# Kernel tuning notes

Hardware: AMD Instinct MI355X
Metric: run time of the kernel (lower is better)

Reference implementation:

```python
import jax, jax.numpy as jnp
import numpy as np

IN_F, OUT_F, RANK, ALPHA, NUM_ADAPTERS = 1024, 1024, 8, 1.0, 8
B, S = 32, 1024
SCALE = ALPHA / RANK


def setup_inputs() -> dict:
    key = jax.random.key(0)
    k1, k2, k3, k4, k5, k6 = jax.random.split(key, 6)
    x = jax.random.normal(k1, (B, S, IN_F), dtype=jnp.float32)
    subject_id = jax.random.randint(k2, (B,), 0, NUM_ADAPTERS)
    # base linear: W [out,in], bias [out] (torch nn.Linear layout)
    W = jax.random.normal(k3, (OUT_F, IN_F), dtype=jnp.float32) * (1.0 / np.sqrt(IN_F))
    b = jax.random.normal(k4, (OUT_F,), dtype=jnp.float32) * 0.01
    # stacked LoRA weights: A [E, rank, in], Bw [E, out, rank]
    # (original inits Bw to zeros; randomized here so the LoRA path is exercised)
    A = jax.random.normal(k5, (NUM_ADAPTERS, RANK, IN_F), dtype=jnp.float32) * 0.02
    Bw = jax.random.normal(k6, (NUM_ADAPTERS, OUT_F, RANK), dtype=jnp.float32) * 0.02
    return {"x": x, "W": W, "b": b, "A": A, "Bw": Bw, "subject_id": subject_id}


def reference(x, W, b, A, Bw, subject_id):
    # base linear: [B,S,O]
    out = jnp.einsum("bsd,od->bso", x, W) + b
    # gather per-batch adapter weights (equivalent to the per-adapter mask loop)
    A_sel = A[subject_id]   # [B, rank, in]
    B_sel = Bw[subject_id]  # [B, out, rank]
    h = jnp.einsum("bsd,brd->bsr", x, A_sel)          # [B,S,rank]
    lora = jnp.einsum("bsr,bor->bso", h, B_sel) * SCALE  # [B,S,out]
    return out + lora
```

## Files before the change

### kernel.cpp

```cpp
#include <hip/hip_runtime.h>
#include <hip/hip_bf16.h>

typedef __bf16 bf16_t;
typedef bf16_t bf16x4 __attribute__((ext_vector_type(4)));
typedef bf16_t bf16x8 __attribute__((ext_vector_type(8)));
typedef float  f32x4  __attribute__((ext_vector_type(4)));

#define IN_F   1024
#define OUT_F  1024
#define RANK   8
#define NE     8
#define BATCH  32
#define SEQ    1024
#define M_TOT  (BATCH * SEQ)
#define SCALE  0.125f
#define NT     16

#define GLOAD_LDS16(g, l)                                                     \
  __builtin_amdgcn_global_load_lds(                                           \
      (const __attribute__((address_space(1))) void*)(g),                     \
      (__attribute__((address_space(3))) void*)(l), 16, 0, 0)

#define CFENCE asm volatile("" ::: "memory")
#define BAR()                                                                 \
  do { CFENCE; __builtin_amdgcn_s_barrier(); CFENCE; } while (0)
#define VMCNT(n) asm volatile("s_waitcnt vmcnt(" #n ")" ::: "memory")
#define LGKM0()  asm volatile("s_waitcnt lgkmcnt(0)" ::: "memory")

__global__ __launch_bounds__(256) void build_weff(
    const float* __restrict__ W, const float* __restrict__ A,
    const float* __restrict__ Bw, bf16_t* __restrict__ weff) {
  const int e  = blockIdx.x >> 10;
  const int o  = blockIdx.x & 1023;
  const int d0 = threadIdx.x << 2;

  f32x4 acc = *(const f32x4*)(W + ((size_t)o << 10) + d0);
  const float* bwr = Bw + (((size_t)e << 10) + o) * RANK;
  const float* ab  = A + (((size_t)e * RANK) << 10) + d0;
#pragma unroll
  for (int r = 0; r < RANK; ++r) {
    const float s = SCALE * bwr[r];
    const f32x4 a4 = *(const f32x4*)(ab + ((size_t)r << 10));
    acc += s * a4;
  }
  bf16x4 ov;
#pragma unroll
  for (int j = 0; j < 4; ++j) ov[j] = (bf16_t)acc[j];
  *(bf16x4*)(weff + (((size_t)e << 10) + o) * IN_F + d0) = ov;
}

__global__ __launch_bounds__(512, 2) void gemm_fused(
    const float* __restrict__ xf, const bf16_t* __restrict__ weff,
    const float* __restrict__ bias, const int* __restrict__ sid,
    float* __restrict__ out) {
  __shared__ bf16_t lds[2][2][2][8192];

  const int bid0 = blockIdx.x;
  const int wgid = ((bid0 & 7) << 6) + (bid0 >> 3);
  const int mb = wgid >> 2, nb = wgid & 3;
  const int m0 = mb << 8, n0 = nb << 8;
  const int e = sid[mb >> 2];

  const int tid = threadIdx.x;
  const int lane = tid & 63, wid = tid >> 6;
  const int wm = wid >> 2, wn = wid & 3;

  const float*  agf   = xf + ((size_t)m0 << 10);
  const bf16_t* bgbase = weff + ((size_t)e << 20) + ((size_t)n0 << 10);

  int soff[2];
#pragma unroll
  for (int i = 0; i < 2; ++i) {
    const int r = (wid << 5) + (i << 4) + (lane >> 2);
    const int sg = (lane & 3) ^ ((r >> 1) & 3);
    soff[i] = (r << 10) + (sg << 3);
  }

  int agoff[4], awoff[4];
  {
    const int c0 = (tid & 7) << 3;
    const int kh = c0 >> 5;
    const int cg = (c0 >> 3) & 3;
#pragma unroll
    for (int q = 0; q < 4; ++q) {
      const int r = (q << 6) + (tid >> 3);
      agoff[q] = (r << 10) + c0;
      const int gs = cg ^ ((r >> 1) & 3);
      awoff[q] = (kh << 13) + (r << 5) + (gs << 3);
    }
  }

  int aoff[8], boff[4];
#pragma unroll
  for (int mi = 0; mi < 8; ++mi) {
    const int r = (wm << 7) + (mi << 4) + (lane & 15);
    const int g = (lane >> 4) ^ ((r >> 1) & 3);
    aoff[mi] = (r << 5) + (g << 3);
  }
#pragma unroll
  for (int ni = 0; ni < 4; ++ni) {
    const int r = (wn << 6) + (ni << 4) + (lane & 15);
    const int g = (lane >> 4) ^ ((r >> 1) & 3);
    boff[ni] = (r << 5) + (g << 3);
  }

  f32x4 acc[8][4] = {};
  f32x4 ar[8];

#define A_ISSUE(kt)                                                           \
  do {                                                                        \
    const float* _x = agf + ((kt) << 6);                                      \
    _Pragma("unroll") for (int q = 0; q < 4; ++q) {                           \
      ar[2 * q]     = *(const f32x4*)(_x + agoff[q]);                         \
      ar[2 * q + 1] = *(const f32x4*)(_x + agoff[q] + 4);                     \
    }                                                                         \
  } while (0)

#define A_WRITE(kt)                                                           \
  do {                                                                        \
    bf16_t* _ab = &lds[(kt) & 1][0][0][0];                                    \
    _Pragma("unroll") for (int q = 0; q < 4; ++q) {                           \
      bf16x8 v;                                                               \
      _Pragma("unroll") for (int i2 = 0; i2 < 4; ++i2) {                      \
        v[i2]     = (bf16_t)ar[2 * q][i2];                                    \
        v[4 + i2] = (bf16_t)ar[2 * q + 1][i2];                                \
      }                                                                       \
      *(bf16x8*)(_ab + awoff[q]) = v;                                         \
    }                                                                         \
  } while (0)

#define BSTAGE(kt, kh)                                                        \
  do {                                                                        \
    bf16_t* _d = &lds[(kt) & 1][1][kh][wid << 10];                            \
    const int _kc = ((kt) << 6) + ((kh) << 5);                                \
    GLOAD_LDS16(bgbase + _kc + soff[0], _d);                                  \
    GLOAD_LDS16(bgbase + _kc + soff[1], _d + 512);                            \
  } while (0)

#define PHASE_READS(kt, kh)                                                   \
  do {                                                                        \
    const bf16_t* _ab = &lds[(kt) & 1][0][kh][0];                             \
    const bf16_t* _bb = &lds[(kt) & 1][1][kh][0];                             \
    _Pragma("unroll") for (int mi = 0; mi < 8; ++mi)                          \
        af[mi] = *(const bf16x8*)(_ab + aoff[mi]);                            \
    _Pragma("unroll") for (int ni = 0; ni < 4; ++ni)                          \
        bfr[ni] = *(const bf16x8*)(_bb + boff[ni]);                           \
  } while (0)

#define MFMAS()                                                               \
  do {                                                                        \
    __builtin_amdgcn_s_setprio(1);                                            \
    _Pragma("unroll") for (int mi = 0; mi < 8; ++mi)                          \
        _Pragma("unroll") for (int ni = 0; ni < 4; ++ni)                      \
            acc[mi][ni] = __builtin_amdgcn_mfma_f32_16x16x32_bf16(            \
                af[mi], bfr[ni], acc[mi][ni], 0, 0, 0);                       \
    __builtin_amdgcn_s_setprio(0);                                            \
  } while (0)

  A_ISSUE(0);
  BSTAGE(0, 0); BSTAGE(0, 1);
  A_WRITE(0);
  A_ISSUE(1);
  BSTAGE(1, 0);
  VMCNT(10);
  LGKM0();
  BAR();

  bf16x8 af[8], bfr[4];
  for (int j = 0; j < NT - 2; ++j) {
    PHASE_READS(j, 0);
    A_WRITE(j + 1);
    A_ISSUE(j + 2);
    BSTAGE(j + 1, 1);
    BAR();
    MFMAS();
    BAR();
    PHASE_READS(j, 1);
    BSTAGE(j + 2, 0);
    VMCNT(2);
    LGKM0();
    BAR();
    MFMAS();
    BAR();
  }
  PHASE_READS(NT - 2, 0);
  A_WRITE(NT - 1);
  BSTAGE(NT - 1, 1);
  BAR();
  MFMAS();
  BAR();
  PHASE_READS(NT - 2, 1);
  VMCNT(0);
  LGKM0();
  BAR();
  MFMAS();
  BAR();
  PHASE_READS(NT - 1, 0);
  MFMAS();
  PHASE_READS(NT - 1, 1);
  MFMAS();

  const int R0 = m0 + (wm << 7);
  const int C0 = n0 + (wn << 6);
  const int crow = (lane >> 4) << 2;
  const int ccol = lane & 15;
#pragma unroll
  for (int ni = 0; ni < 4; ++ni) {
    const int col = C0 + (ni << 4) + ccol;
    const float bv = bias[col];
#pragma unroll
    for (int mi = 0; mi < 8; ++mi) {
      const int row = R0 + (mi << 4) + crow;
#pragma unroll
      for (int j2 = 0; j2 < 4; ++j2)
        out[((size_t)(row + j2) << 10) + col] = acc[mi][ni][j2] + bv;
    }
  }
#undef A_ISSUE
#undef A_WRITE
#undef BSTAGE
#undef PHASE_READS
#undef MFMAS
}

__global__ __launch_bounds__(256) void lora_naive(
    const float* __restrict__ x, const float* __restrict__ W,
    const float* __restrict__ bias, const float* __restrict__ A,
    const float* __restrict__ Bw, const int* __restrict__ sid,
    float* __restrict__ out) {
  const int m = blockIdx.x;
  const int e = sid[m >> 10];
  __shared__ float xs[IN_F];
  __shared__ float h[RANK];
  const int tid = threadIdx.x;
  for (int i = tid; i < IN_F; i += 256) xs[i] = x[((size_t)m << 10) + i];
  __syncthreads();
  if (tid < RANK) {
    float s = 0.f;
    const float* ar = A + (((size_t)e * RANK + tid) << 10);
    for (int d = 0; d < IN_F; ++d) s += xs[d] * ar[d];
    h[tid] = s * SCALE;
  }
  __syncthreads();
  for (int o = tid; o < OUT_F; o += 256) {
    const float* wr = W + ((size_t)o << 10);
    float s = 0.f;
    for (int d = 0; d < IN_F; ++d) s += xs[d] * wr[d];
    const float* bwr = Bw + (((size_t)e << 10) + o) * RANK;
    float l = 0.f;
#pragma unroll
    for (int r = 0; r < RANK; ++r) l += h[r] * bwr[r];
    out[((size_t)m << 10) + o] = s + bias[o] + l;
  }
}

extern "C" void kernel_launch(void* const* d_in, const int* in_sizes, int n_in,
                              void* d_out, int out_size, void* d_ws,
                              size_t ws_size, hipStream_t stream) {
  const float* x   = (const float*)d_in[0];
  const float* W   = (const float*)d_in[1];
  const float* b   = (const float*)d_in[2];
  const float* A   = (const float*)d_in[3];
  const float* Bw  = (const float*)d_in[4];
  const int*   sid = (const int*)d_in[5];
  float* out = (float*)d_out;

  const size_t weff_bytes = (size_t)NE * OUT_F * IN_F * 2;

  if (ws_size >= weff_bytes) {
    bf16_t* weff = (bf16_t*)d_ws;
    hipLaunchKernelGGL(build_weff, dim3(NE * OUT_F), dim3(256), 0, stream,
                       W, A, Bw, weff);
    hipLaunchKernelGGL(gemm_fused, dim3((M_TOT / 256) * (OUT_F / 256)),
                       dim3(512), 0, stream, x, weff, b, sid, out);
  } else {
    hipLaunchKernelGGL(lora_naive, dim3(M_TOT), dim3(256), 0, stream,
                       x, W, b, A, Bw, sid, out);
  }
}
```

Before: 119.8 us.

## Restructure A LDS tile to full-row 64-wide XOR swizzle and reorder async loads

Result: slower. 123.5 us (+3.1%).

```diff
diff --git a/kernel.cpp b/kernel.cpp
--- a/kernel.cpp
+++ b/kernel.cpp
@@ -53,7 +53,8 @@
     const float* __restrict__ xf, const bf16_t* __restrict__ weff,
     const float* __restrict__ bias, const int* __restrict__ sid,
     float* __restrict__ out) {
-  __shared__ bf16_t lds[2][2][2][8192];
+  __shared__ bf16_t lds_a[2][16384];
+  __shared__ bf16_t lds_b[2][2][8192];
 
   const int bid0 = blockIdx.x;
   const int wgid = ((bid0 & 7) << 6) + (bid0 >> 3);
@@ -65,7 +66,7 @@
   const int lane = tid & 63, wid = tid >> 6;
   const int wm = wid >> 2, wn = wid & 3;
 
-  const float*  agf   = xf + ((size_t)m0 << 10);
+  const float*  agf    = xf + ((size_t)m0 << 10);
   const bf16_t* bgbase = weff + ((size_t)e << 20) + ((size_t)n0 << 10);
 
   int soff[2];
@@ -78,24 +79,23 @@
 
   int agoff[4], awoff[4];
   {
-    const int c0 = (tid & 7) << 3;
-    const int kh = c0 >> 5;
-    const int cg = (c0 >> 3) & 3;
+    const int c = tid & 7;
 #pragma unroll
     for (int q = 0; q < 4; ++q) {
       const int r = (q << 6) + (tid >> 3);
-      agoff[q] = (r << 10) + c0;
-      const int gs = cg ^ ((r >> 1) & 3);
-      awoff[q] = (kh << 13) + (r << 5) + (gs << 3);
+      agoff[q] = (r << 10) + (c << 3);
+      awoff[q] = (r << 6) + ((c ^ (r & 7)) << 3);
     }
   }
 
-  int aoff[8], boff[4];
+  int aoff0[8], aoff1[8], boff[4];
 #pragma unroll
   for (int mi = 0; mi < 8; ++mi) {
     const int r = (wm << 7) + (mi << 4) + (lane & 15);
-    const int g = (lane >> 4) ^ ((r >> 1) & 3);
-    aoff[mi] = (r << 5) + (g << 3);
+    const int g0 = (lane >> 4) ^ (r & 7);
+    const int g1 = (4 + (lane >> 4)) ^ (r & 7);
+    aoff0[mi] = (r << 6) + (g0 << 3);
+    aoff1[mi] = (r << 6) + (g1 << 3);
   }
 #pragma unroll
   for (int ni = 0; ni < 4; ++ni) {
@@ -118,7 +118,7 @@
 
 #define A_WRITE(kt)                                                           \
   do {                                                                        \
-    bf16_t* _ab = &lds[(kt) & 1][0][0][0];                                    \
+    bf16_t* _ab = &lds_a[(kt) & 1][0];                                        \
     _Pragma("unroll") for (int q = 0; q < 4; ++q) {                           \
       bf16x8 v;                                                               \
       _Pragma("unroll") for (int i2 = 0; i2 < 4; ++i2) {                      \
@@ -131,7 +131,7 @@
 
 #define BSTAGE(kt, kh)                                                        \
   do {                                                                        \
-    bf16_t* _d = &lds[(kt) & 1][1][kh][wid << 10];                            \
+    bf16_t* _d = &lds_b[(kt) & 1][kh][wid << 10];                             \
     const int _kc = ((kt) << 6) + ((kh) << 5);                                \
     GLOAD_LDS16(bgbase + _kc + soff[0], _d);                                  \
     GLOAD_LDS16(bgbase + _kc + soff[1], _d + 512);                            \
@@ -139,10 +139,10 @@
 
 #define PHASE_READS(kt, kh)                                                   \
   do {                                                                        \
-    const bf16_t* _ab = &lds[(kt) & 1][0][kh][0];                             \
-    const bf16_t* _bb = &lds[(kt) & 1][1][kh][0];                             \
+    const bf16_t* _ab = &lds_a[(kt) & 1][0];                                  \
+    const bf16_t* _bb = &lds_b[(kt) & 1][kh][0];                              \
     _Pragma("unroll") for (int mi = 0; mi < 8; ++mi)                          \
-        af[mi] = *(const bf16x8*)(_ab + aoff[mi]);                            \
+        af[mi] = *(const bf16x8*)(_ab + ((kh) ? aoff1[mi] : aoff0[mi]));      \
     _Pragma("unroll") for (int ni = 0; ni < 4; ++ni)                          \
         bfr[ni] = *(const bf16x8*)(_bb + boff[ni]);                           \
   } while (0)
@@ -162,7 +162,7 @@
   A_WRITE(0);
   A_ISSUE(1);
   BSTAGE(1, 0);
-  VMCNT(10);
+  VMCNT(12);
   LGKM0();
   BAR();
 
@@ -170,14 +170,14 @@
   for (int j = 0; j < NT - 2; ++j) {
     PHASE_READS(j, 0);
     A_WRITE(j + 1);
+    BSTAGE(j + 1, 1);
     A_ISSUE(j + 2);
-    BSTAGE(j + 1, 1);
     BAR();
     MFMAS();
     BAR();
     PHASE_READS(j, 1);
     BSTAGE(j + 2, 0);
-    VMCNT(2);
+    VMCNT(12);
     LGKM0();
     BAR();
     MFMAS();
```
